# Optimization experiments

Measured on AMD Instinct MI355X. Metric: run time of the kernel, lower is better.

The kernel has to match this reference:

```python
import jax, jax.numpy as jnp
import numpy as np

W_, N_, C_, E_ = 12, 20000, 64, 320000
HOPS_ = 2
DIL_ = 1
KERNELS = (1, 3, 5, 7)


def setup_inputs() -> dict:
    key = jax.random.key(0)
    ks = jax.random.split(key, 32)
    inp = {
        "x": jax.random.normal(ks[0], (W_, N_, C_), jnp.float32),
        "edge_index": jax.random.randint(ks[1], (W_, 2, E_), 0, N_, dtype=jnp.int32),
        "edge_weight": jax.random.uniform(ks[2], (W_, E_), jnp.float32),
    }
    cout4 = C_ // len(KERNELS)
    ki = 3
    for k in KERNELS:
        inp[f"sw{k}"] = jax.random.normal(ks[ki], (cout4, C_, k), jnp.float32) * 0.05; ki += 1
        inp[f"sb{k}"] = jax.random.normal(ks[ki], (cout4,), jnp.float32) * 0.05; ki += 1
        inp[f"gw{k}"] = jax.random.normal(ks[ki], (cout4, C_, k), jnp.float32) * 0.05; ki += 1
        inp[f"gb{k}"] = jax.random.normal(ks[ki], (cout4,), jnp.float32) * 0.05; ki += 1
    # distinct GCN weights per (hop, time-step), as in nn.ModuleList of ModuleLists
    inp["gcn_w"] = jax.random.normal(ks[ki], (HOPS_, W_, C_, C_), jnp.float32) * 0.05
    inp["gcn_b"] = jax.random.normal(ks[ki + 1], (HOPS_, W_, C_), jnp.float32) * 0.05
    return inp


def _inception(x_ncw, ws, bs):
    # x_ncw: [N, C, W]; 'same'-length dilated conv1d per kernel, concat on channels
    outs = []
    for w, b, k in zip(ws, bs, KERNELS):
        p = DIL_ * (k - 1) // 2
        y = jax.lax.conv_general_dilated(
            x_ncw, w, window_strides=(1,), padding=[(p, p)],
            rhs_dilation=(DIL_,), dimension_numbers=("NCH", "OIH", "NCH"))
        outs.append(y + b[None, :, None])
    return jnp.concatenate(outs, axis=1)  # [N, Cout, W]


def reference(x, edge_index, edge_weight,
              sw1, sb1, sw3, sb3, sw5, sb5, sw7, sb7,
              gw1, gb1, gw3, gb3, gw5, gb5, gw7, gb7,
              gcn_w, gcn_b):
    n = x.shape[1]
    # ---- temporal block (temporal_first=True) ----
    xt = x.transpose(1, 2, 0)  # [N, C, W]
    sig = _inception(xt, (sw1, sw3, sw5, sw7), (sb1, sb3, sb5, sb7))
    gate = _inception(xt, (gw1, gw3, gw5, gw7), (gb1, gb3, gb5, gb7))
    h = jax.nn.relu(sig) * jax.nn.sigmoid(gate)  # [N, Cout, W]
    h = h.transpose(2, 0, 1)  # [W, N, Cout]

    # ---- spatial block: num_hops GCNConv(normalize=False) + ELU per time step ----
    src = edge_index[:, 0]  # [W, E]
    dst = edge_index[:, 1]  # [W, E]

    def gcn_step(hw, s, d, ew, w, b):
        # GCNConv, normalize=False: scatter-add of ew * (x @ W)[src] onto dst, + bias
        m = ew[:, None] * (hw @ w)[s]                      # [E, C]
        agg = jax.ops.segment_sum(m, d, num_segments=n)    # [N, C]
        return jax.nn.elu(agg + b)

    for j in range(gcn_w.shape[0]):
        h = jax.vmap(gcn_step)(h, src, dst, edge_weight, gcn_w[j], gcn_b[j])

    # ---- residual add (identity; residualConn is unused in the torch forward) ----
    return h + x
```

## Files before the change

### kernel.cpp

```cpp
#include <hip/hip_runtime.h>
#include <hip/hip_fp16.h>
#include <cstddef>

#define Wn 12
#define Nn 20000
#define Cn 64
#define En 320000
#define OFFS_STRIDE 20032
#define NBKT 79
#define BCAP 4672

typedef _Float16 h4v __attribute__((ext_vector_type(4)));
typedef _Float16 h8v __attribute__((ext_vector_type(8)));
typedef float    f4v __attribute__((ext_vector_type(4)));

__device__ __forceinline__ float elu_f(float v) {
    return v > 0.f ? v : (expf(v) - 1.f);
}

__global__ __launch_bounds__(256) void wprep_kernel(
    const float* __restrict__ sw1, const float* __restrict__ gw1,
    const float* __restrict__ sw3, const float* __restrict__ gw3,
    const float* __restrict__ sw5, const float* __restrict__ gw5,
    const float* __restrict__ sw7, const float* __restrict__ gw7,
    __half* __restrict__ dst)
{
    const int i = blockIdx.x * 256 + threadIdx.x;
    if (i >= 32768) return;
    const int j    = i & 7;
    const int lane = (i >> 3) & 63;
    const int slot = i >> 9;
    int g, loc;
    if (slot < 4)       { g = 0; loc = slot; }
    else if (slot < 16) { g = 1; loc = slot - 4; }
    else if (slot < 36) { g = 2; loc = slot - 16; }
    else                { g = 3; loc = slot - 36; }
    const int k   = 2 * g + 1;
    const int nks = 2 * k;
    const int sg  = (loc >= nks) ? 1 : 0;
    const int s   = loc - sg * nks;
    const int t   = s >> 1;
    const int ih  = s & 1;
    const int oc  = lane & 15;
    const int ic  = ih * 32 + (lane >> 4) * 8 + j;
    const float* src;
    switch (g * 2 + sg) {
      case 0: src = sw1; break; case 1: src = gw1; break;
      case 2: src = sw3; break; case 3: src = gw3; break;
      case 4: src = sw5; break; case 5: src = gw5; break;
      case 6: src = sw7; break; default: src = gw7; break;
    }
    dst[i] = __float2half(src[(oc * 64 + ic) * k + t]);
}

__global__ __launch_bounds__(256) void gwprep_kernel(
    const float* __restrict__ gcnw, __half* __restrict__ dst)
{
    const int i = blockIdx.x * 256 + threadIdx.x;
    if (i >= 98304) return;
    const int j      = i & 7;
    const int lane   = (i >> 3) & 63;
    const int kh     = (i >> 9) & 1;
    const int octile = (i >> 10) & 3;
    const int hw     = i >> 12;
    const int ic = (lane >> 4) * 8 + j + kh * 32;
    const int oc = octile * 16 + (lane & 15);
    dst[i] = __float2half(gcnw[(size_t)hw * 4096 + ic * 64 + oc]);
}

template<int G>
__device__ __forceinline__ void mfma_group(
    const __half* __restrict__ wTg,
    const __half* __restrict__ xsh,
    const float* __restrict__ sb, const float* __restrict__ gb,
    float* __restrict__ h, int nb, int tid)
{
    constexpr int NKS = 2 * (2 * G + 1);
    const int lane = tid & 63;
    const int wv   = tid >> 6;
    const int node16 = lane & 15;
    const int abase = node16 * 128;
    const int swz   = (lane & 7) << 4;
    const int aoff0 = abase + ((0  + (lane >> 4) * 16) ^ swz);
    const int aoff1 = abase + ((64 + (lane >> 4) * 16) ^ swz);

    f4v accS[3], accG[3];
    #pragma unroll
    for (int m = 0; m < 3; ++m) {
        accS[m] = (f4v){0.f, 0.f, 0.f, 0.f};
        accG[m] = (f4v){0.f, 0.f, 0.f, 0.f};
    }

    #pragma unroll
    for (int s2 = 0; s2 < 2 * G + 1; ++s2) {
        const int dw = s2 - G;
        #pragma unroll
        for (int ih = 0; ih < 2; ++ih) {
            const int s = s2 * 2 + ih;
            const h8v bs = *(const h8v*)&wTg[(s * 64 + lane) * 8];
            const h8v bg = *(const h8v*)&wTg[((NKS + s) * 64 + lane) * 8];
            const int laneoff = ih ? aoff1 : aoff0;
            #pragma unroll
            for (int m = 0; m < 3; ++m) {
                const int w  = wv * 3 + m;
                const int wp = w + dw;
                if (wp >= 0 && wp < Wn) {
                    const h8v a = *(const h8v*)((const char*)xsh + wp * 2048 + laneoff);
                    accS[m] = __builtin_amdgcn_mfma_f32_16x16x32_f16(a, bs, accS[m], 0, 0, 0);
                    accG[m] = __builtin_amdgcn_mfma_f32_16x16x32_f16(a, bg, accG[m], 0, 0, 0);
                }
            }
        }
    }

    const float sbv = sb[node16];
    const float gbv = gb[node16];
    const int oc = G * 16 + node16;
    #pragma unroll
    for (int m = 0; m < 3; ++m) {
        const int w = wv * 3 + m;
        #pragma unroll
        for (int r = 0; r < 4; ++r) {
            const int node = (lane >> 4) * 4 + r;
            const float sv = accS[m][r] + sbv;
            const float gv = accG[m][r] + gbv;
            const float rv = sv > 0.f ? sv : 0.f;
            const float sg = 1.f / (1.f + expf(-gv));
            h[((size_t)w * Nn + nb + node) * Cn + oc] = rv * sg;
        }
    }
}

__global__ __launch_bounds__(256, 4) void inception_mfma_kernel(
    const float* __restrict__ x,
    const float* __restrict__ sb1, const float* __restrict__ gb1,
    const float* __restrict__ sb3, const float* __restrict__ gb3,
    const float* __restrict__ sb5, const float* __restrict__ gb5,
    const float* __restrict__ sb7, const float* __restrict__ gb7,
    const __half* __restrict__ wT,
    float* __restrict__ h)
{
    __shared__ __align__(16) __half xsh[12 * 16 * 64];
    const int tid = threadIdx.x;
    const int nb  = blockIdx.x * 16;

    const float4* xg = (const float4*)x;
    for (int i = tid; i < 3072; i += 256) {
        const int w = i >> 8, r = i & 255, node = r >> 4, c4 = r & 15;
        const float4 v = xg[((size_t)w * Nn + nb + node) * 16 + c4];
        h4v p = { (_Float16)v.x, (_Float16)v.y, (_Float16)v.z, (_Float16)v.w };
        const int off = w * 2048 + node * 128 + (((c4 << 3)) ^ ((node & 7) << 4));
        *(h4v*)((char*)xsh + off) = p;
    }
    __syncthreads();
    mfma_group<0>(wT,         xsh, sb1, gb1, h, nb, tid);
    mfma_group<1>(wT + 2048,  xsh, sb3, gb3, h, nb, tid);
    mfma_group<2>(wT + 8192,  xsh, sb5, gb5, h, nb, tid);
    mfma_group<3>(wT + 18432, xsh, sb7, gb7, h, nb, tid);
}

__global__ __launch_bounds__(256) void mm_mfma_kernel(
    const float* __restrict__ h, const __half* __restrict__ gwp,
    __half* __restrict__ t)
{
    __shared__ __align__(16) __half hsh[64 * 64];
    const int w   = blockIdx.y;
    const int nb  = blockIdx.x * 64;
    const int tid = threadIdx.x;

    const float4* hg = (const float4*)h;
    #pragma unroll
    for (int p = 0; p < 4; ++p) {
        const int i2 = tid + p * 256;
        const int node = i2 >> 4, c4 = i2 & 15;
        const int nclamp = (nb + node < Nn) ? (nb + node) : (Nn - 1);
        const float4 v = hg[((size_t)w * Nn + nclamp) * 16 + c4];
        h4v pk = { (_Float16)v.x, (_Float16)v.y, (_Float16)v.z, (_Float16)v.w };
        const int off = node * 128 + (((c4 << 3)) ^ ((node & 7) << 4));
        *(h4v*)((char*)hsh + off) = pk;
    }
    __syncthreads();

    const int lane = tid & 63;
    const int wv   = tid >> 6;
    const int abase = (wv * 16 + (lane & 15)) * 128;
    const int swz   = (lane & 7) << 4;
    const h8v a0 = *(const h8v*)((const char*)hsh + abase + ((0  + (lane >> 4) * 16) ^ swz));
    const h8v a1 = *(const h8v*)((const char*)hsh + abase + ((64 + (lane >> 4) * 16) ^ swz));

    const int node0 = nb + wv * 16 + (lane >> 4) * 4;
    #pragma unroll
    for (int ot = 0; ot < 4; ++ot) {
        const h8v b0 = *(const h8v*)&gwp[(((w * 4 + ot) * 2 + 0) * 64 + lane) * 8];
        const h8v b1 = *(const h8v*)&gwp[(((w * 4 + ot) * 2 + 1) * 64 + lane) * 8];
        f4v acc = (f4v){0.f, 0.f, 0.f, 0.f};
        acc = __builtin_amdgcn_mfma_f32_16x16x32_f16(a0, b0, acc, 0, 0, 0);
        acc = __builtin_amdgcn_mfma_f32_16x16x32_f16(a1, b1, acc, 0, 0, 0);
        const int oc = ot * 16 + (lane & 15);
        #pragma unroll
        for (int r = 0; r < 4; ++r) {
            const int node = node0 + r;
            if (node < Nn)
                t[((size_t)w * Nn + node) * Cn + oc] = __float2half(acc[r]);
        }
    }
}

__global__ __launch_bounds__(256) void bucketA_kernel(
    const int* __restrict__ ei, const float* __restrict__ ew,
    int* __restrict__ bcur, uint2* __restrict__ bstr)
{
    const int w   = blockIdx.y;
    const int tid = threadIdx.x;
    __shared__ uint2 compact[2560];
    __shared__ unsigned char bkid[2560];
    __shared__ int rcnt[NBKT], rbase[NBKT], sbase[NBKT];
    __shared__ int sc[128];

    const int* eis = ei + (size_t)w * 2 * En;
    const float* ews = ew + (size_t)w * En;
    const int e0 = blockIdx.x * 2560;

    if (tid < NBKT) rcnt[tid] = 0;
    __syncthreads();

    int myb[10], myr[10];
    uint2 mye[10];
    #pragma unroll
    for (int it = 0; it < 10; ++it) {
        const int e = e0 + it * 256 + tid;
        const int s = eis[e];
        const int d = eis[En + e];
        const float wt = ews[e];
        const int bk = d >> 8;
        myb[it] = bk;
        mye[it].x = (unsigned)s | ((unsigned)(d & 255) << 16);
        mye[it].y = __float_as_uint(wt);
        myr[it] = atomicAdd(&rcnt[bk], 1);
    }
    __syncthreads();
    if (tid < 128) sc[tid] = (tid < NBKT) ? rcnt[tid] : 0;
    __syncthreads();
    #pragma unroll
    for (int dlt = 1; dlt < 128; dlt <<= 1) {
        int t = (tid < 128 && tid >= dlt) ? sc[tid - dlt] : 0;
        __syncthreads();
        if (tid < 128) sc[tid] += t;
        __syncthreads();
    }
    if (tid < NBKT) {
        rbase[tid] = sc[tid] - rcnt[tid];
        sbase[tid] = atomicAdd(&bcur[w * 80 + tid], rcnt[tid]);
    }
    __syncthreads();
    #pragma unroll
    for (int it = 0; it < 10; ++it) {
        const int p = rbase[myb[it]] + myr[it];
        compact[p] = mye[it];
        bkid[p] = (unsigned char)myb[it];
    }
    __syncthreads();
    for (int i = tid; i < 2560; i += 256) {
        const int bk = bkid[i];
        int off = sbase[bk] + (i - rbase[bk]);
        if (off >= BCAP) off = BCAP - 1;
        bstr[((size_t)w * NBKT + bk) * BCAP + off] = compact[i];
    }
}

__global__ __launch_bounds__(768) void bscan_kernel(
    const int* __restrict__ bcur, int* __restrict__ bbase)
{
    const int lane = threadIdx.x & 63;
    const int w    = threadIdx.x >> 6;
    const int c0 = (lane < NBKT) ? bcur[w * 80 + lane] : 0;
    int s = c0;
    #pragma unroll
    for (int d = 1; d < 64; d <<= 1) {
        int t = __shfl_up(s, d);
        if (lane >= d) s += t;
    }
    const int tot0 = __shfl(s, 63);
    const int c1 = (lane + 64 < NBKT) ? bcur[w * 80 + 64 + lane] : 0;
    int s1 = c1;
    #pragma unroll
    for (int d = 1; d < 64; d <<= 1) {
        int t = __shfl_up(s1, d);
        if (lane >= d) s1 += t;
    }
    s1 += tot0;
    bbase[w * 80 + lane] = s - c0;
    if (lane + 64 < NBKT) bbase[w * 80 + 64 + lane] = s1 - c1;
}

__global__ __launch_bounds__(256) void bucketB_kernel(
    const uint2* __restrict__ bstr, const int* __restrict__ bcur,
    const int* __restrict__ bbase, int* __restrict__ offs,
    float2* __restrict__ pairs)
{
    const int bk = blockIdx.x, w = blockIdx.y;
    const int tid = threadIdx.x;
    __shared__ uint2 sorted[BCAP];
    __shared__ int lhist[256], lbase[256], wsum[4];
    int n = bcur[w * 80 + bk];
    if (n > BCAP) n = BCAP;
    const int gbase = bbase[w * 80 + bk];
    const uint2* src = bstr + ((size_t)w * NBKT + bk) * BCAP;

    lhist[tid] = 0;
    __syncthreads();

    constexpr int MAXE = (BCAP + 255) / 256;
    uint2 mye[MAXE];
    short myd[MAXE], myr[MAXE];
    #pragma unroll
    for (int it = 0; it < MAXE; ++it) {
        const int i = tid + it * 256;
        if (i < n) {
            const uint2 e = src[i];
            mye[it] = e;
            const int dl = (e.x >> 16) & 255;
            myd[it] = (short)dl;
            myr[it] = (short)atomicAdd(&lhist[dl], 1);
        }
    }
    __syncthreads();
    {
        const int lane = tid & 63, wv = tid >> 6;
        const int v = lhist[tid];
        int sum = v;
        #pragma unroll
        for (int dlt = 1; dlt < 64; dlt <<= 1) {
            int t = __shfl_up(sum, dlt);
            if (lane >= dlt) sum += t;
        }
        if (lane == 63) wsum[wv] = sum;
        __syncthreads();
        if (tid < 4) {
            int o = wsum[tid], s2 = o;
            #pragma unroll
            for (int dlt = 1; dlt < 4; dlt <<= 1) {
                int t = __shfl_up(s2, dlt);
                if (tid >= dlt) s2 += t;
            }
            wsum[tid] = s2 - o;
        }
        __syncthreads();
        const int be = wsum[wv] + sum - v;
        lbase[tid] = be;
        const int d = bk * 256 + tid;
        if (d < Nn) offs[w * OFFS_STRIDE + d] = gbase + be;
        if (bk == NBKT - 1 && tid == 0) offs[w * OFFS_STRIDE + Nn] = En;
    }
    __syncthreads();
    #pragma unroll
    for (int it = 0; it < MAXE; ++it) {
        const int i = tid + it * 256;
        if (i < n)
            sorted[lbase[myd[it]] + myr[it]] = mye[it];
    }
    __syncthreads();
    float2* pw = pairs + (size_t)w * En + gbase;
    for (int i = tid; i < n; i += 256) {
        const uint2 e = sorted[i];
        pw[i] = make_float2(__int_as_float((int)(e.x & 0xFFFFu)), __uint_as_float(e.y));
    }
}

template<bool LAST>
__global__ __launch_bounds__(256) void agg_kernel(
    const __half* __restrict__ t, const float2* __restrict__ pairs,
    const int* __restrict__ offs, const float* __restrict__ b,
    const float* __restrict__ x, float* __restrict__ out)
{
    const int blk = blockIdx.x;
    const int r = blk & 7, q = blk >> 3;
    int w, ng;
    if (q < 5000) { w = r; ng = q; }
    else { int q2 = q - 5000; w = 8 + (r >> 1); ng = q2 * 2 + (r & 1); }

    const int d    = ng * 4 + (threadIdx.x >> 6);
    const int lane = threadIdx.x & 63;
    const int eg   = lane >> 4;
    const int c4   = lane & 15;
    const int* ow  = offs + w * OFFS_STRIDE;
    const int beg = ow[d];
    const int end = ow[d + 1];
    const float2* pw = pairs + (size_t)w * En;
    const __half* tw = t + (size_t)w * Nn * Cn;

    float a0 = 0.f, a1 = 0.f, a2 = 0.f, a3 = 0.f;
    int i = beg;
    for (; i + 8 <= end; i += 8) {
        const float2 pA = pw[i + eg];
        const float2 pB = pw[i + 4 + eg];
        const uint2 rA = *(const uint2*)&tw[(size_t)__float_as_int(pA.x) * Cn + c4 * 4];
        const uint2 rB = *(const uint2*)&tw[(size_t)__float_as_int(pB.x) * Cn + c4 * 4];
        const float2 fa01 = __half22float2(*(const __half2*)&rA.x);
        const float2 fa23 = __half22float2(*(const __half2*)&rA.y);
        const float2 fb01 = __half22float2(*(const __half2*)&rB.x);
        const float2 fb23 = __half22float2(*(const __half2*)&rB.y);
        a0 = fmaf(pA.y, fa01.x, a0);
        a1 = fmaf(pA.y, fa01.y, a1);
        a2 = fmaf(pA.y, fa23.x, a2);
        a3 = fmaf(pA.y, fa23.y, a3);
        a0 = fmaf(pB.y, fb01.x, a0);
        a1 = fmaf(pB.y, fb01.y, a1);
        a2 = fmaf(pB.y, fb23.x, a2);
        a3 = fmaf(pB.y, fb23.y, a3);
    }
    if (i + 4 <= end) {
        const float2 pA = pw[i + eg];
        const uint2 rA = *(const uint2*)&tw[(size_t)__float_as_int(pA.x) * Cn + c4 * 4];
        const float2 fa01 = __half22float2(*(const __half2*)&rA.x);
        const float2 fa23 = __half22float2(*(const __half2*)&rA.y);
        a0 = fmaf(pA.y, fa01.x, a0);
        a1 = fmaf(pA.y, fa01.y, a1);
        a2 = fmaf(pA.y, fa23.x, a2);
        a3 = fmaf(pA.y, fa23.y, a3);
        i += 4;
    }
    if (i + eg < end) {
        const float2 pA = pw[i + eg];
        const uint2 rA = *(const uint2*)&tw[(size_t)__float_as_int(pA.x) * Cn + c4 * 4];
        const float2 fa01 = __half22float2(*(const __half2*)&rA.x);
        const float2 fa23 = __half22float2(*(const __half2*)&rA.y);
        a0 = fmaf(pA.y, fa01.x, a0);
        a1 = fmaf(pA.y, fa01.y, a1);
        a2 = fmaf(pA.y, fa23.x, a2);
        a3 = fmaf(pA.y, fa23.y, a3);
    }

    a0 += __shfl_xor(a0, 16); a0 += __shfl_xor(a0, 32);
    a1 += __shfl_xor(a1, 16); a1 += __shfl_xor(a1, 32);
    a2 += __shfl_xor(a2, 16); a2 += __shfl_xor(a2, 32);
    a3 += __shfl_xor(a3, 16); a3 += __shfl_xor(a3, 32);

    if (eg == 0) {
        const float4 bv = *(const float4*)&b[w * Cn + c4 * 4];
        float v0 = elu_f(a0 + bv.x);
        float v1 = elu_f(a1 + bv.y);
        float v2 = elu_f(a2 + bv.z);
        float v3 = elu_f(a3 + bv.w);
        const size_t oi = ((size_t)w * Nn + d) * Cn + c4 * 4;
        if (LAST) {
            const float4 xv = *(const float4*)&x[oi];
            v0 += xv.x; v1 += xv.y; v2 += xv.z; v3 += xv.w;
        }
        *(float4*)&out[oi] = make_float4(v0, v1, v2, v3);
    }
}

extern "C" void kernel_launch(void* const* d_in, const int* in_sizes, int n_in,
                              void* d_out, int out_size, void* d_ws, size_t ws_size,
                              hipStream_t stream)
{
    const float* x    = (const float*)d_in[0];
    const int*   ei   = (const int*)d_in[1];
    const float* ew   = (const float*)d_in[2];
    const float* sw1  = (const float*)d_in[3];
    const float* sb1  = (const float*)d_in[4];
    const float* gw1  = (const float*)d_in[5];
    const float* gb1  = (const float*)d_in[6];
    const float* sw3  = (const float*)d_in[7];
    const float* sb3  = (const float*)d_in[8];
    const float* gw3  = (const float*)d_in[9];
    const float* gb3  = (const float*)d_in[10];
    const float* sw5  = (const float*)d_in[11];
    const float* sb5  = (const float*)d_in[12];
    const float* gw5  = (const float*)d_in[13];
    const float* gb5  = (const float*)d_in[14];
    const float* sw7  = (const float*)d_in[15];
    const float* sb7  = (const float*)d_in[16];
    const float* gw7  = (const float*)d_in[17];
    const float* gb7  = (const float*)d_in[18];
    const float* gcnw = (const float*)d_in[19];
    const float* gcnb = (const float*)d_in[20];
    float* out = (float*)d_out;
    __half* Th = (__half*)d_out;

    const size_t WNC = (size_t)Wn * Nn * Cn;
    const int mm_grid = (Nn + 63) / 64;

    float2* pairs = (float2*)d_ws;
    int*    offs  = (int*)((float*)d_ws + 7680000);
    int*    bcur  = offs + 240384;
    int*    bbase = bcur + 1024;
    __half* wT    = (__half*)(bcur + 240000);
    __half* gwp   = wT + 32768;
    float*  H     = (float*)((int*)(bcur + 240000) + 240000);
    uint2*  bstr  = (uint2*)H;

    hipMemsetAsync(bcur, 0, (size_t)Wn * 80 * sizeof(int), stream);
    bucketA_kernel<<<dim3(En / 2560, Wn), 256, 0, stream>>>(ei, ew, bcur, bstr);
    bscan_kernel<<<1, 768, 0, stream>>>(bcur, bbase);
    bucketB_kernel<<<dim3(NBKT, Wn), 256, 0, stream>>>(bstr, bcur, bbase, offs, pairs);

    wprep_kernel<<<128, 256, 0, stream>>>(sw1, gw1, sw3, gw3, sw5, gw5, sw7, gw7, wT);
    gwprep_kernel<<<384, 256, 0, stream>>>(gcnw, gwp);

    inception_mfma_kernel<<<Nn / 16, 256, 0, stream>>>(
        x, sb1, gb1, sb3, gb3, sb5, gb5, sb7, gb7, wT, H);

    mm_mfma_kernel<<<dim3(mm_grid, Wn), 256, 0, stream>>>(H, gwp, Th);
    agg_kernel<false><<<60000, 256, 0, stream>>>(
        Th, pairs, offs, gcnb, nullptr, H);

    mm_mfma_kernel<<<dim3(mm_grid, Wn), 256, 0, stream>>>(
        H, gwp + (size_t)Wn * 4096, Th);
    agg_kernel<true><<<60000, 256, 0, stream>>>(
        Th, pairs, offs, gcnb + (size_t)Wn * Cn, x, H);
    hipMemcpyAsync(out, H, WNC * sizeof(float), hipMemcpyDeviceToDevice, stream);
}
```

Measured before the change: 556.4 us.

## Batch gather loads in GCN aggregation and load MFMA operands directly from global

The GCN aggregation loop now issues up to eight edge-pair loads and eight row gathers per lane before any FMA, raising memory-level parallelism in the latency-bound gather. The tail handling is folded into predicated iterations. Separately, the MFMA matmul kernel drops its LDS staging and barrier and loads each lane's A fragment straight from global memory with float4 reads. The cost is more registers in the gather kernel and uncoalesced per-lane row loads in the matmul.

```diff
diff --git a/kernel.cpp b/kernel.cpp
--- a/kernel.cpp
+++ b/kernel.cpp
@@ -163,30 +163,23 @@
     const float* __restrict__ h, const __half* __restrict__ gwp,
     __half* __restrict__ t)
 {
-    __shared__ __align__(16) __half hsh[64 * 64];
-    const int w   = blockIdx.y;
-    const int nb  = blockIdx.x * 64;
-    const int tid = threadIdx.x;
-
-    const float4* hg = (const float4*)h;
-    #pragma unroll
-    for (int p = 0; p < 4; ++p) {
-        const int i2 = tid + p * 256;
-        const int node = i2 >> 4, c4 = i2 & 15;
-        const int nclamp = (nb + node < Nn) ? (nb + node) : (Nn - 1);
-        const float4 v = hg[((size_t)w * Nn + nclamp) * 16 + c4];
-        h4v pk = { (_Float16)v.x, (_Float16)v.y, (_Float16)v.z, (_Float16)v.w };
-        const int off = node * 128 + (((c4 << 3)) ^ ((node & 7) << 4));
-        *(h4v*)((char*)hsh + off) = pk;
-    }
-    __syncthreads();
-
+    const int w    = blockIdx.y;
+    const int nb   = blockIdx.x * 64;
+    const int tid  = threadIdx.x;
     const int lane = tid & 63;
     const int wv   = tid >> 6;
-    const int abase = (wv * 16 + (lane & 15)) * 128;
-    const int swz   = (lane & 7) << 4;
-    const h8v a0 = *(const h8v*)((const char*)hsh + abase + ((0  + (lane >> 4) * 16) ^ swz));
-    const h8v a1 = *(const h8v*)((const char*)hsh + abase + ((64 + (lane >> 4) * 16) ^ swz));
+    const int node = nb + wv * 16 + (lane & 15);
+    const int nc   = (node < Nn) ? node : (Nn - 1);
+    const float* hrow = h + ((size_t)w * Nn + nc) * 64 + (lane >> 4) * 8;
+
+    const float4 q0a = *(const float4*)&hrow[0];
+    const float4 q0b = *(const float4*)&hrow[4];
+    const float4 q1a = *(const float4*)&hrow[32];
+    const float4 q1b = *(const float4*)&hrow[36];
+    const h8v a0 = { (_Float16)q0a.x, (_Float16)q0a.y, (_Float16)q0a.z, (_Float16)q0a.w,
+                     (_Float16)q0b.x, (_Float16)q0b.y, (_Float16)q0b.z, (_Float16)q0b.w };
+    const h8v a1 = { (_Float16)q1a.x, (_Float16)q1a.y, (_Float16)q1a.z, (_Float16)q1a.w,
+                     (_Float16)q1b.x, (_Float16)q1b.y, (_Float16)q1b.z, (_Float16)q1b.w };
 
     const int node0 = nb + wv * 16 + (lane >> 4) * 4;
     #pragma unroll
@@ -199,9 +192,9 @@
         const int oc = ot * 16 + (lane & 15);
         #pragma unroll
         for (int r = 0; r < 4; ++r) {
-            const int node = node0 + r;
-            if (node < Nn)
-                t[((size_t)w * Nn + node) * Cn + oc] = __float2half(acc[r]);
+            const int nd = node0 + r;
+            if (nd < Nn)
+                t[((size_t)w * Nn + nd) * Cn + oc] = __float2half(acc[r]);
         }
     }
 }
@@ -387,48 +380,36 @@
     const int beg = ow[d];
     const int end = ow[d + 1];
     const float2* pw = pairs + (size_t)w * En;
-    const __half* tw = t + (size_t)w * Nn * Cn;
+    const __half* twc = t + (size_t)w * Nn * Cn + c4 * 4;
 
     float a0 = 0.f, a1 = 0.f, a2 = 0.f, a3 = 0.f;
-    int i = beg;
-    for (; i + 8 <= end; i += 8) {
-        const float2 pA = pw[i + eg];
-        const float2 pB = pw[i + 4 + eg];
-        const uint2 rA = *(const uint2*)&tw[(size_t)__float_as_int(pA.x) * Cn + c4 * 4];
-        const uint2 rB = *(const uint2*)&tw[(size_t)__float_as_int(pB.x) * Cn + c4 * 4];
-        const float2 fa01 = __half22float2(*(const __half2*)&rA.x);
-        const float2 fa23 = __half22float2(*(const __half2*)&rA.y);
-        const float2 fb01 = __half22float2(*(const __half2*)&rB.x);
-        const float2 fb23 = __half22float2(*(const __half2*)&rB.y);
-        a0 = fmaf(pA.y, fa01.x, a0);
-        a1 = fmaf(pA.y, fa01.y, a1);
-        a2 = fmaf(pA.y, fa23.x, a2);
-        a3 = fmaf(pA.y, fa23.y, a3);
-        a0 = fmaf(pB.y, fb01.x, a0);
-        a1 = fmaf(pB.y, fb01.y, a1);
-        a2 = fmaf(pB.y, fb23.x, a2);
-        a3 = fmaf(pB.y, fb23.y, a3);
-    }
-    if (i + 4 <= end) {
-        const float2 pA = pw[i + eg];
-        const uint2 rA = *(const uint2*)&tw[(size_t)__float_as_int(pA.x) * Cn + c4 * 4];
-        const float2 fa01 = __half22float2(*(const __half2*)&rA.x);
-        const float2 fa23 = __half22float2(*(const __half2*)&rA.y);
-        a0 = fmaf(pA.y, fa01.x, a0);
-        a1 = fmaf(pA.y, fa01.y, a1);
-        a2 = fmaf(pA.y, fa23.x, a2);
-        a3 = fmaf(pA.y, fa23.y, a3);
-        i += 4;
-    }
-    if (i + eg < end) {
-        const float2 pA = pw[i + eg];
-        const uint2 rA = *(const uint2*)&tw[(size_t)__float_as_int(pA.x) * Cn + c4 * 4];
-        const float2 fa01 = __half22float2(*(const __half2*)&rA.x);
-        const float2 fa23 = __half22float2(*(const __half2*)&rA.y);
-        a0 = fmaf(pA.y, fa01.x, a0);
-        a1 = fmaf(pA.y, fa01.y, a1);
-        a2 = fmaf(pA.y, fa23.x, a2);
-        a3 = fmaf(pA.y, fa23.y, a3);
+
+    for (int base = beg; base < end; base += 32) {
+        float2 p[8];
+        #pragma unroll
+        for (int jj = 0; jj < 8; ++jj) {
+            const int idx = base + jj * 4 + eg;
+            if (idx < end) p[jj] = pw[idx];
+        }
+        uint2 rr[8];
+        #pragma unroll
+        for (int jj = 0; jj < 8; ++jj) {
+            const int idx = base + jj * 4 + eg;
+            if (idx < end)
+                rr[jj] = *(const uint2*)(twc + (size_t)__float_as_int(p[jj].x) * Cn);
+        }
+        #pragma unroll
+        for (int jj = 0; jj < 8; ++jj) {
+            const int idx = base + jj * 4 + eg;
+            if (idx < end) {
+                const float2 f01 = __half22float2(*(const __half2*)&rr[jj].x);
+                const float2 f23 = __half22float2(*(const __half2*)&rr[jj].y);
+                a0 = fmaf(p[jj].y, f01.x, a0);
+                a1 = fmaf(p[jj].y, f01.y, a1);
+                a2 = fmaf(p[jj].y, f23.x, a2);
+                a3 = fmaf(p[jj].y, f23.y, a3);
+            }
+        }
     }
 
     a0 += __shfl_xor(a0, 16); a0 += __shfl_xor(a0, 32);
```

New measurement: 600.0 us. 7.8% more time.
